# Optimization experiments

Hardware: AMD Instinct MI355X
Metric: run time of the kernel (lower is better)

## Reference

```python
import jax, jax.numpy as jnp
import numpy as np

B, L, D = 8, 4096, 1024
EPS = 1e-6


def setup_inputs() -> dict:
    key = jax.random.key(0)
    k1, k2, k3 = jax.random.split(key, 3)
    x = jax.random.normal(k1, (B, L, D), dtype=jnp.float32)
    # torch.nn.Linear default init ~ U(-1/sqrt(d), 1/sqrt(d)); scaled normal is fine for a reference
    w_in = jax.random.normal(k2, (3 * D, D), dtype=jnp.float32) * (D ** -0.5)
    w_out = jax.random.normal(k3, (D, D), dtype=jnp.float32) * (D ** -0.5)
    scale = jnp.ones((D,), dtype=jnp.float32)
    return {"x": x, "w_in": w_in, "w_out": w_out, "scale": scale}


def reference(x, w_in, w_out, scale):
    residual = x
    # RMSNorm: ||x||_2 * d^{-1/2}
    norm = jnp.linalg.norm(x, axis=-1, keepdims=True) * (x.shape[-1] ** -0.5)
    xn = scale * x / (norm + EPS)
    # proj_in: Linear(d, 3d, bias=False) -> chunk into g, v, f
    gvf = jnp.einsum('bld,ed->ble', xn, w_in)  # [B, L, 3D]
    g, v, f = jnp.split(gvf, 3, axis=-1)
    g = jax.nn.sigmoid(g)
    f = jax.nn.sigmoid(f - 1.0)

    # sequential gated linear recurrence: h_t = f_t * h_{t-1} + (1 - f_t) * v_t
    def step(h, fv):
        ft, vt = fv  # each [B, D]
        h = ft * h + (1.0 - ft) * vt
        return h, h

    h0 = jnp.zeros((x.shape[0], x.shape[2]), dtype=x.dtype)
    _, h_seq = jax.lax.scan(step, h0, (jnp.swapaxes(f, 0, 1), jnp.swapaxes(v, 0, 1)))
    h_seq = jnp.swapaxes(h_seq, 0, 1)  # [B, L, D]

    out = g * h_seq
    return residual + jnp.einsum('bld,ed->ble', out, w_out)
```

## Files before the change

### kernel.cpp

```cpp
#include <hip/hip_runtime.h>
#include <cstdint>
#include <cstddef>

typedef unsigned short u16;
typedef __attribute__((ext_vector_type(8))) short short8;
typedef __attribute__((ext_vector_type(4))) float floatx4;
typedef __attribute__((ext_vector_type(4))) unsigned short ushort4v;

constexpr int D_ = 1024;
constexpr int B_ = 8;
constexpr int L_ = 4096;
constexpr int M_ = B_ * L_;
constexpr int NCHUNK = 64;
constexpr int CLEN = L_ / NCHUNK;
constexpr float EPS_ = 1e-6f;
constexpr size_t WIN_ELEMS = (size_t)3 * D_ * D_;
constexpr size_t WOUT_ELEMS = (size_t)D_ * D_;
constexpr int NT_K = 16;
constexpr int PREPW_BLOCKS = (int)((WIN_ELEMS + WOUT_ELEMS) / 8 / 256);

__device__ __forceinline__ float bf2f(u16 b) {
    union { unsigned u; float f; } x; x.u = ((unsigned)b) << 16; return x.f;
}
__device__ __forceinline__ u16 f2bf(float f) {
    union { float f; unsigned u; } x; x.f = f;
    unsigned r = x.u + 0x7fffu + ((x.u >> 16) & 1u);
    return (u16)(r >> 16);
}
__device__ __forceinline__ float sigmoidf_(float x) {
    return 1.f / (1.f + __expf(-x));
}
__device__ __forceinline__ short8 cvt8(const float* __restrict__ p) {
    float4 a = *(const float4*)p;
    float4 b = *(const float4*)(p + 4);
    short8 o;
    o[0] = (short)f2bf(a.x); o[1] = (short)f2bf(a.y);
    o[2] = (short)f2bf(a.z); o[3] = (short)f2bf(a.w);
    o[4] = (short)f2bf(b.x); o[5] = (short)f2bf(b.y);
    o[6] = (short)f2bf(b.z); o[7] = (short)f2bf(b.w);
    return o;
}
__device__ __forceinline__ void gload16(const void* g, void* l) {
    __builtin_amdgcn_global_load_lds((const __attribute__((address_space(1))) void*)g,
                                     (__attribute__((address_space(3))) void*)l, 16, 0, 0);
}

__global__ __launch_bounds__(256) void prep_kernel(const float* __restrict__ x,
                                                   const float* __restrict__ scale,
                                                   u16* __restrict__ xn,
                                                   const float* __restrict__ w_in,
                                                   const float* __restrict__ w_out,
                                                   u16* __restrict__ w_in_bf,
                                                   u16* __restrict__ w_out_bf) {
    const int t = threadIdx.x;
    if ((int)blockIdx.x >= M_) {
        size_t i8 = ((size_t)(blockIdx.x - M_) * 256 + t) * 8;
        if (i8 < WIN_ELEMS) {
            *(short8*)(w_in_bf + i8) = cvt8(w_in + i8);
        } else {
            size_t j = i8 - WIN_ELEMS;
            *(short8*)(w_out_bf + j) = cvt8(w_out + j);
        }
        return;
    }
    const int row = blockIdx.x;
    const float* xr = x + (size_t)row * D_;
    float4 xv = ((const float4*)xr)[t];
    float ss = xv.x * xv.x + xv.y * xv.y + xv.z * xv.z + xv.w * xv.w;
#pragma unroll
    for (int m = 32; m >= 1; m >>= 1) ss += __shfl_xor(ss, m, 64);
    __shared__ float red[4];
    const int wave = t >> 6, lane = t & 63;
    if (lane == 0) red[wave] = ss;
    __syncthreads();
    float tot = red[0] + red[1] + red[2] + red[3];
    float inv = 1.f / (sqrtf(tot * (1.f / D_)) + EPS_);
    float4 sv = ((const float4*)scale)[t];
    ushort4v o;
    o[0] = f2bf(xv.x * inv * sv.x);
    o[1] = f2bf(xv.y * inv * sv.y);
    o[2] = f2bf(xv.z * inv * sv.z);
    o[3] = f2bf(xv.w * inv * sv.w);
    ((ushort4v*)(xn + (size_t)row * D_))[t] = o;
}


#define STAGE_A_(buf, half, koff) do { \
    const u16* g_ = gA0 + (koff) + (half) * 65536; \
    u16* l_ = (buf) + ((half) * 64 + iw) * 64; \
    gload16(g_, l_); gload16(g_ + 131072, l_ + 8192); } while (0)
#define STAGE_B_(buf, half, koff) do { \
    const u16* g_ = gB0 + (koff) + (half) * 32768; \
    u16* l_ = (buf) + (rBw + (half) * 32) * 64; \
    gload16(g_, l_); gload16(g_ + 131072, l_ + 8192); } while (0)
#define BARRIER_() do { __builtin_amdgcn_sched_barrier(0); \
    __builtin_amdgcn_s_barrier(); \
    __builtin_amdgcn_sched_barrier(0); } while (0)
#define LDA4_(mlo) do { \
    _Pragma("unroll") for (int m_ = 0; m_ < 4; ++m_) { \
      int o_ = aOff + ((mlo) + m_) * 2048; \
      af[m_][0] = *(const short8*)((const char*)curA + o_); \
      af[m_][1] = *(const short8*)((const char*)curA + (o_ ^ 64)); } } while (0)
#define LDB2_(nlo) do { \
    _Pragma("unroll") for (int n_ = 0; n_ < 2; ++n_) { \
      int o_ = bOff + ((nlo) + n_) * 2048; \
      bfv[(nlo) + n_][0] = *(const short8*)((const char*)curB + o_); \
      bfv[(nlo) + n_][1] = *(const short8*)((const char*)curB + (o_ ^ 64)); } } while (0)
#define MFMA_Q_(mlo, nlo) do { \
    __builtin_amdgcn_s_setprio(1); \
    _Pragma("unroll") for (int m_ = 0; m_ < 4; ++m_) \
    _Pragma("unroll") for (int n_ = 0; n_ < 2; ++n_) \
    _Pragma("unroll") for (int k_ = 0; k_ < 2; ++k_) \
      acc[(mlo) + m_][(nlo) + n_] = __builtin_amdgcn_mfma_f32_16x16x32_bf16( \
          af[m_][k_], bfv[(nlo) + n_][k_], acc[(mlo) + m_][(nlo) + n_], 0, 0, 0); \
    __builtin_amdgcn_s_setprio(0); } while (0)

__device__ __forceinline__ void tile_step(int tt, u16* curA, u16* curB, u16* othA, u16* othB,
                                          const u16* gA0, const u16* gB0, int iw, int rBw,
                                          int aOff, int bOff, floatx4 (&acc)[8][4]) {
    short8 af[4][2], bfv[4][2];
    const int k1 = (tt + 1) * 64, k2 = (tt + 2) * 64;
    const bool s1 = (tt + 1 < NT_K), s2 = (tt + 2 < NT_K);
    LDA4_(0); LDB2_(0); LDB2_(2);
    if (s1) { STAGE_A_(othA, 1, k1); STAGE_B_(othB, 1, k1); }
    MFMA_Q_(0, 0);
    MFMA_Q_(0, 2);
    BARRIER_();
    LDA4_(4);
    if (s2) { STAGE_A_(curA, 0, k2); STAGE_B_(curB, 0, k2); }
    MFMA_Q_(4, 0);
    MFMA_Q_(4, 2);
    if (s2)      { asm volatile("s_waitcnt vmcnt(4)" ::: "memory"); }
    else if (s1) { asm volatile("s_waitcnt vmcnt(0)" ::: "memory"); }
    BARRIER_();
}

__device__ __forceinline__ void gemm256_core(const u16* __restrict__ gA,
                                             const u16* __restrict__ gB,
                                             int m0, int n0,
                                             u16* __restrict__ As, u16* __restrict__ Bs,
                                             floatx4 (&acc)[8][4]) {
    const int t = threadIdx.x;
    const int wid = t >> 6, lane = t & 63;
    const int wr = wid >> 2, wc = wid & 3;
    const int l15 = lane & 15, quad = lane >> 4;
    const int jrow = lane >> 3, jc = lane & 7;
    const int swz = ((jc ^ (jrow & 7)) << 3);
    const u16* gA0 = gA + (size_t)(m0 + wid * 8 + jrow) * 1024 + swz;
    const int i0 = wid * 8 + jrow;
    const int rB0 = ((i0 >> 5) << 6) + (i0 & 31);
    const u16* gB0 = gB + (size_t)(n0 + rB0) * 1024 + swz;
    const int iw = wid * 8;
    const int rBw = ((iw >> 5) << 6) + (iw & 31);
    const int c0 = (quad * 16) ^ ((l15 & 7) << 4);
    const int aOff = (wr * 128 + l15) * 128 + c0;
    const int bOff = (wc * 64 + l15) * 128 + c0;

#pragma unroll
    for (int i = 0; i < 8; i++)
#pragma unroll
        for (int j = 0; j < 4; j++) { floatx4 z = {0.f, 0.f, 0.f, 0.f}; acc[i][j] = z; }

    STAGE_A_(As, 0, 0); STAGE_A_(As, 1, 0);
    STAGE_B_(Bs, 0, 0); STAGE_B_(Bs, 1, 0);
    STAGE_A_(As + 16384, 0, 64);
    STAGE_B_(Bs + 16384, 0, 64);
    asm volatile("s_waitcnt vmcnt(4)" ::: "memory");
    BARRIER_();

#pragma unroll 1
    for (int tt = 0; tt < NT_K; tt += 2) {
        tile_step(tt,     As,         Bs,         As + 16384, Bs + 16384,
                  gA0, gB0, iw, rBw, aOff, bOff, acc);
        tile_step(tt + 1, As + 16384, Bs + 16384, As,         Bs,
                  gA0, gB0, iw, rBw, aOff, bOff, acc);
    }
}

__global__ __launch_bounds__(512, 2) void gemm1_kernel(const u16* __restrict__ xn,
                                                       const u16* __restrict__ w_in,
                                                       u16* __restrict__ g_buf,
                                                       u16* __restrict__ v_buf,
                                                       u16* __restrict__ f_buf) {
    __shared__ __align__(16) u16 SH[65536];
    const int m0 = blockIdx.y * 256;
    const int n0 = blockIdx.x * 256;
    floatx4 acc[8][4];
    gemm256_core(xn, w_in, m0, n0, SH, SH + 32768, acc);

    const int t = threadIdx.x;
    const int wid = t >> 6, lane = t & 63;
    const int wr = wid >> 2, wc = wid & 3;
    const int l15 = lane & 15, quad = lane >> 4;
    const int plane = n0 >> 10;
    const int cbase = n0 & 1023;
    u16* dst = (plane == 0) ? g_buf : ((plane == 1) ? v_buf : f_buf);

#pragma unroll
    for (int mt = 0; mt < 8; mt++) {
#pragma unroll
        for (int r = 0; r < 4; r++) {
            int row = wr * 128 + mt * 16 + quad * 4 + r;
            int xr = (row & 7) << 3;
#pragma unroll
            for (int nt = 0; nt < 4; nt++) {
                int colb = (wc * 64 + nt * 16 + l15) * 2;
                float val = acc[mt][nt][r];
                if (plane == 0) val = sigmoidf_(val);
                else if (plane == 2) val = sigmoidf_(val - 1.f);
                *(u16*)((char*)SH + row * 512 + (colb ^ xr)) = f2bf(val);
            }
        }
    }
    __syncthreads();
    const int lane8 = lane * 8;
#pragma unroll 4
    for (int i = 0; i < 32; i++) {
        int row = wid + i * 8;
        int xr = (row & 7) << 3;
        uint2 v = *(const uint2*)((const char*)SH + row * 512 + (lane8 ^ xr));
        *(uint2*)(dst + (size_t)(m0 + row) * 1024 + cbase + lane * 4) = v;
    }
}

__global__ __launch_bounds__(512, 2) void gemm2_kernel(const u16* __restrict__ op,
                                                       const u16* __restrict__ w_out,
                                                       const float* __restrict__ xres,
                                                       float* __restrict__ out) {
    __shared__ __align__(16) u16 SH[65536];
    const int m0 = blockIdx.y * 256;
    const int n0 = blockIdx.x * 256;
    floatx4 acc[8][4];
    gemm256_core(op, w_out, m0, n0, SH, SH + 32768, acc);

    const int t = threadIdx.x;
    const int wid = t >> 6, lane = t & 63;
    const int wr = wid >> 2, wc = wid & 3;
    const int l15 = lane & 15, quad = lane >> 4;
    const int ncol0 = n0 + wc * 64;
    const int mrow0 = m0 + wr * 128 + quad * 4;
#pragma unroll
    for (int mt = 0; mt < 8; mt++) {
#pragma unroll
        for (int r = 0; r < 4; r++) {
            int m = mrow0 + mt * 16 + r;
#pragma unroll
            for (int nt = 0; nt < 4; nt++) {
                size_t idx = (size_t)m * 1024 + ncol0 + nt * 16 + l15;
                out[idx] = acc[mt][nt][r] + xres[idx];
            }
        }
    }
}

__global__ __launch_bounds__(256) void scan1_kernel(const u16* __restrict__ f_buf,
                                                    const u16* __restrict__ v_buf,
                                                    float* __restrict__ Aarr,
                                                    float* __restrict__ Barr) {
    const int wid = blockIdx.x * 4 + (threadIdx.x >> 6);
    const int lane = threadIdx.x & 63;
    const int b = wid >> 8;
    const int rem = wid & 255;
    const int c = rem >> 2;
    const int d0 = (rem & 3) * 256 + lane * 4;
    float A[4], Bv[4];
#pragma unroll
    for (int j = 0; j < 4; j++) { A[j] = 1.f; Bv[j] = 0.f; }
    size_t base = ((size_t)b * L_ + c * CLEN) * D_ + d0;
#pragma unroll 2
    for (int tt = 0; tt < CLEN; tt++) {
        ushort4v f4 = *(const ushort4v*)(f_buf + base + (size_t)tt * D_);
        ushort4v v4 = *(const ushort4v*)(v_buf + base + (size_t)tt * D_);
#pragma unroll
        for (int j = 0; j < 4; j++) {
            float fv = bf2f(f4[j]);
            float vv = bf2f(v4[j]);
            A[j] *= fv;
            Bv[j] = fv * Bv[j] + (1.f - fv) * vv;
        }
    }
    size_t sidx = ((size_t)b * NCHUNK + c) * D_ + d0;
    floatx4 oA = {A[0], A[1], A[2], A[3]};
    floatx4 oB = {Bv[0], Bv[1], Bv[2], Bv[3]};
    *(floatx4*)(Aarr + sidx) = oA;
    *(floatx4*)(Barr + sidx) = oB;
}

__global__ __launch_bounds__(256) void scan2_kernel(const float* __restrict__ Aarr,
                                                    const float* __restrict__ Barr,
                                                    float* __restrict__ hin) {
    const int id = blockIdx.x * 256 + threadIdx.x;
    const int b = id >> 8, d0 = (id & 255) * 4;
    float h[4] = {0.f, 0.f, 0.f, 0.f};
    for (int c = 0; c < NCHUNK; c++) {
        size_t idx = ((size_t)b * NCHUNK + c) * D_ + d0;
        floatx4 oh = {h[0], h[1], h[2], h[3]};
        *(floatx4*)(hin + idx) = oh;
        floatx4 a = *(const floatx4*)(Aarr + idx);
        floatx4 bb = *(const floatx4*)(Barr + idx);
#pragma unroll
        for (int j = 0; j < 4; j++) h[j] = a[j] * h[j] + bb[j];
    }
}

__global__ __launch_bounds__(256) void scan3_kernel(const u16* __restrict__ f_buf,
                                                    const u16* __restrict__ v_buf,
                                                    u16* g_io,
                                                    const float* __restrict__ hin) {
    const int wid = blockIdx.x * 4 + (threadIdx.x >> 6);
    const int lane = threadIdx.x & 63;
    const int b = wid >> 8;
    const int rem = wid & 255;
    const int c = rem >> 2;
    const int d0 = (rem & 3) * 256 + lane * 4;
    size_t base = ((size_t)b * L_ + c * CLEN) * D_ + d0;
    floatx4 hv = *(const floatx4*)(hin + ((size_t)b * NCHUNK + c) * D_ + d0);
    float h[4] = {hv[0], hv[1], hv[2], hv[3]};
#pragma unroll 2
    for (int tt = 0; tt < CLEN; tt++) {
        size_t idx = base + (size_t)tt * D_;
        ushort4v f4 = *(const ushort4v*)(f_buf + idx);
        ushort4v v4 = *(const ushort4v*)(v_buf + idx);
        ushort4v g4 = *(const ushort4v*)(g_io + idx);
        ushort4v o;
#pragma unroll
        for (int j = 0; j < 4; j++) {
            float fv = bf2f(f4[j]);
            float vv = bf2f(v4[j]);
            float gv = bf2f(g4[j]);
            h[j] = fv * h[j] + (1.f - fv) * vv;
            o[j] = f2bf(gv * h[j]);
        }
        *(ushort4v*)(g_io + idx) = o;
    }
}

extern "C" void kernel_launch(void* const* d_in, const int* in_sizes, int n_in,
                              void* d_out, int out_size, void* d_ws, size_t ws_size,
                              hipStream_t stream) {
    const float* x     = (const float*)d_in[0];
    const float* w_in  = (const float*)d_in[1];
    const float* w_out = (const float*)d_in[2];
    const float* scale = (const float*)d_in[3];
    float* out = (float*)d_out;

    u16* f_buf = (u16*)d_out;
    u16* v_buf = (u16*)d_out + (size_t)M_ * D_;

    char* ws = (char*)d_ws;
    const size_t PLANE = (size_t)M_ * D_ * sizeof(u16);
    u16* xn    = (u16*)ws;
    u16* g_buf = (u16*)(ws + PLANE);
    u16* w_in_bf  = (u16*)(ws + 2 * PLANE);
    u16* w_out_bf = w_in_bf + WIN_ELEMS;
    float* Aarr = (float*)(ws + 2 * PLANE + (WIN_ELEMS + WOUT_ELEMS) * sizeof(u16));
    float* Barr = Aarr + (size_t)B_ * NCHUNK * D_;
    float* hin  = Barr + (size_t)B_ * NCHUNK * D_;

    prep_kernel<<<M_ + PREPW_BLOCKS, 256, 0, stream>>>(x, scale, xn, w_in, w_out,
                                                       w_in_bf, w_out_bf);
    gemm1_kernel<<<dim3(3 * D_ / 256, M_ / 256), 512, 0, stream>>>(
        xn, w_in_bf, g_buf, v_buf, f_buf);
    scan1_kernel<<<512, 256, 0, stream>>>(f_buf, v_buf, Aarr, Barr);
    scan2_kernel<<<8, 256, 0, stream>>>(Aarr, Barr, hin);
    scan3_kernel<<<512, 256, 0, stream>>>(f_buf, v_buf, g_buf, hin);
    gemm2_kernel<<<dim3(D_ / 256, M_ / 256), 512, 0, stream>>>(g_buf, w_out_bf, x, out);
}
```

Before: 614.9 us.

## Remap GEMM blocks per XCD, one-wave-per-row RMSNorm, widen scan parallelism and unrolling

GEMM block indices are remapped so each XCD works on a contiguous band of 16 M-tiles, which should raise L2 reuse of the A rows across N tiles. The RMSNorm prep now handles one row per wave with four rows per block, which removes the shared-memory reduction and barrier. scan2 uses one thread per channel over 32 blocks instead of 8 blocks of float4 threads, giving more parallelism for the serial chunk scan. The scan1 and scan3 loops are unrolled further to raise memory-level parallelism, at the cost of more registers.

```diff
diff --git a/kernel.cpp b/kernel.cpp
--- a/kernel.cpp
+++ b/kernel.cpp
@@ -17,6 +17,7 @@
 constexpr size_t WIN_ELEMS = (size_t)3 * D_ * D_;
 constexpr size_t WOUT_ELEMS = (size_t)D_ * D_;
 constexpr int NT_K = 16;
+constexpr int PREPX_BLOCKS = M_ / 4;
 constexpr int PREPW_BLOCKS = (int)((WIN_ELEMS + WOUT_ELEMS) / 8 / 256);
 
 __device__ __forceinline__ float bf2f(u16 b) {
@@ -53,8 +54,8 @@
                                                    u16* __restrict__ w_in_bf,
                                                    u16* __restrict__ w_out_bf) {
     const int t = threadIdx.x;
-    if ((int)blockIdx.x >= M_) {
-        size_t i8 = ((size_t)(blockIdx.x - M_) * 256 + t) * 8;
+    if ((int)blockIdx.x >= PREPX_BLOCKS) {
+        size_t i8 = ((size_t)(blockIdx.x - PREPX_BLOCKS) * 256 + t) * 8;
         if (i8 < WIN_ELEMS) {
             *(short8*)(w_in_bf + i8) = cvt8(w_in + i8);
         } else {
@@ -63,25 +64,30 @@
         }
         return;
     }
-    const int row = blockIdx.x;
+    const int wave = t >> 6, lane = t & 63;
+    const int row = blockIdx.x * 4 + wave;
     const float* xr = x + (size_t)row * D_;
-    float4 xv = ((const float4*)xr)[t];
-    float ss = xv.x * xv.x + xv.y * xv.y + xv.z * xv.z + xv.w * xv.w;
+    float4 xv[4];
+#pragma unroll
+    for (int j = 0; j < 4; j++) xv[j] = ((const float4*)xr)[lane + j * 64];
+    float ss = 0.f;
+#pragma unroll
+    for (int j = 0; j < 4; j++)
+        ss += xv[j].x * xv[j].x + xv[j].y * xv[j].y + xv[j].z * xv[j].z + xv[j].w * xv[j].w;
 #pragma unroll
     for (int m = 32; m >= 1; m >>= 1) ss += __shfl_xor(ss, m, 64);
-    __shared__ float red[4];
-    const int wave = t >> 6, lane = t & 63;
-    if (lane == 0) red[wave] = ss;
-    __syncthreads();
-    float tot = red[0] + red[1] + red[2] + red[3];
-    float inv = 1.f / (sqrtf(tot * (1.f / D_)) + EPS_);
-    float4 sv = ((const float4*)scale)[t];
-    ushort4v o;
-    o[0] = f2bf(xv.x * inv * sv.x);
-    o[1] = f2bf(xv.y * inv * sv.y);
-    o[2] = f2bf(xv.z * inv * sv.z);
-    o[3] = f2bf(xv.w * inv * sv.w);
-    ((ushort4v*)(xn + (size_t)row * D_))[t] = o;
+    float inv = 1.f / (sqrtf(ss * (1.f / D_)) + EPS_);
+    u16* xo = xn + (size_t)row * D_;
+#pragma unroll
+    for (int j = 0; j < 4; j++) {
+        float4 sv = ((const float4*)scale)[lane + j * 64];
+        ushort4v o;
+        o[0] = f2bf(xv[j].x * inv * sv.x);
+        o[1] = f2bf(xv[j].y * inv * sv.y);
+        o[2] = f2bf(xv[j].z * inv * sv.z);
+        o[3] = f2bf(xv[j].w * inv * sv.w);
+        ((ushort4v*)xo)[lane + j * 64] = o;
+    }
 }
 
 
@@ -177,14 +183,21 @@
     }
 }
 
+__device__ __forceinline__ void xcd_decode(int& m0, int& n0) {
+    const int lid = blockIdx.x;
+    const int xcd = lid & 7, loc = lid >> 3;
+    m0 = (xcd * 16 + (loc & 15)) * 256;
+    n0 = (loc >> 4) * 256;
+}
+
 __global__ __launch_bounds__(512, 2) void gemm1_kernel(const u16* __restrict__ xn,
                                                        const u16* __restrict__ w_in,
                                                        u16* __restrict__ g_buf,
                                                        u16* __restrict__ v_buf,
                                                        u16* __restrict__ f_buf) {
     __shared__ __align__(16) u16 SH[65536];
-    const int m0 = blockIdx.y * 256;
-    const int n0 = blockIdx.x * 256;
+    int m0, n0;
+    xcd_decode(m0, n0);
     floatx4 acc[8][4];
     gemm256_core(xn, w_in, m0, n0, SH, SH + 32768, acc);
 
@@ -228,8 +241,8 @@
                                                        const float* __restrict__ xres,
                                                        float* __restrict__ out) {
     __shared__ __align__(16) u16 SH[65536];
-    const int m0 = blockIdx.y * 256;
-    const int n0 = blockIdx.x * 256;
+    int m0, n0;
+    xcd_decode(m0, n0);
     floatx4 acc[8][4];
     gemm256_core(op, w_out, m0, n0, SH, SH + 32768, acc);
 
@@ -267,7 +280,7 @@
 #pragma unroll
     for (int j = 0; j < 4; j++) { A[j] = 1.f; Bv[j] = 0.f; }
     size_t base = ((size_t)b * L_ + c * CLEN) * D_ + d0;
-#pragma unroll 2
+#pragma unroll 8
     for (int tt = 0; tt < CLEN; tt++) {
         ushort4v f4 = *(const ushort4v*)(f_buf + base + (size_t)tt * D_);
         ushort4v v4 = *(const ushort4v*)(v_buf + base + (size_t)tt * D_);
@@ -290,16 +303,13 @@
                                                     const float* __restrict__ Barr,
                                                     float* __restrict__ hin) {
     const int id = blockIdx.x * 256 + threadIdx.x;
-    const int b = id >> 8, d0 = (id & 255) * 4;
-    float h[4] = {0.f, 0.f, 0.f, 0.f};
+    const int b = id >> 10, d = id & 1023;
+    float h = 0.f;
+#pragma unroll 4
     for (int c = 0; c < NCHUNK; c++) {
-        size_t idx = ((size_t)b * NCHUNK + c) * D_ + d0;
-        floatx4 oh = {h[0], h[1], h[2], h[3]};
-        *(floatx4*)(hin + idx) = oh;
-        floatx4 a = *(const floatx4*)(Aarr + idx);
-        floatx4 bb = *(const floatx4*)(Barr + idx);
-#pragma unroll
-        for (int j = 0; j < 4; j++) h[j] = a[j] * h[j] + bb[j];
+        size_t idx = ((size_t)b * NCHUNK + c) * D_ + d;
+        hin[idx] = h;
+        h = Aarr[idx] * h + Barr[idx];
     }
 }
 
@@ -316,7 +326,7 @@
     size_t base = ((size_t)b * L_ + c * CLEN) * D_ + d0;
     floatx4 hv = *(const floatx4*)(hin + ((size_t)b * NCHUNK + c) * D_ + d0);
     float h[4] = {hv[0], hv[1], hv[2], hv[3]};
-#pragma unroll 2
+#pragma unroll 8
     for (int tt = 0; tt < CLEN; tt++) {
         size_t idx = base + (size_t)tt * D_;
         ushort4v f4 = *(const ushort4v*)(f_buf + idx);
@@ -357,12 +367,11 @@
     float* Barr = Aarr + (size_t)B_ * NCHUNK * D_;
     float* hin  = Barr + (size_t)B_ * NCHUNK * D_;
 
-    prep_kernel<<<M_ + PREPW_BLOCKS, 256, 0, stream>>>(x, scale, xn, w_in, w_out,
-                                                       w_in_bf, w_out_bf);
-    gemm1_kernel<<<dim3(3 * D_ / 256, M_ / 256), 512, 0, stream>>>(
-        xn, w_in_bf, g_buf, v_buf, f_buf);
+    prep_kernel<<<PREPX_BLOCKS + PREPW_BLOCKS, 256, 0, stream>>>(x, scale, xn, w_in, w_out,
+                                                                 w_in_bf, w_out_bf);
+    gemm1_kernel<<<1536, 512, 0, stream>>>(xn, w_in_bf, g_buf, v_buf, f_buf);
     scan1_kernel<<<512, 256, 0, stream>>>(f_buf, v_buf, Aarr, Barr);
-    scan2_kernel<<<8, 256, 0, stream>>>(Aarr, Barr, hin);
+    scan2_kernel<<<32, 256, 0, stream>>>(Aarr, Barr, hin);
     scan3_kernel<<<512, 256, 0, stream>>>(f_buf, v_buf, g_buf, hin);
-    gemm2_kernel<<<dim3(D_ / 256, M_ / 256), 512, 0, stream>>>(g_buf, w_out_bf, x, out);
-}
+    gemm2_kernel<<<512, 512, 0, stream>>>(g_buf, w_out_bf, x, out);
+}
```

Result: slower. 660.6 us (+7.4%).
